# Performance work log

Hardware: AMD Instinct MI355X
Metric: run time of the kernel (lower is better)

The kernel has to match this reference:

```python
import math
import jax, jax.numpy as jnp
import numpy as np

# ---- module hyperparameters (from init_kwargs) ----
N_DELTA, N_THETA, N_GAMMA = 32, 64, 256
N_TOTAL = N_DELTA + N_THETA + N_GAMMA  # 352
N_DIMS = 1024
BATCH = 4096
N_STEPS = 32
DT = 0.01
COUPLING = 2.0
PAC = 0.3
EPS = 1e-6
TWO_PI = 2.0 * math.pi


def setup_inputs() -> dict:
    key = jax.random.key(0)
    k0, k1, k2 = jax.random.split(key, 3)
    x = jax.random.normal(k0, (BATCH, N_DIMS), dtype=jnp.float32)
    # xavier_uniform with gain=0.5 for Linear(n_dims, n_total, bias=False)
    bound = 0.5 * math.sqrt(6.0 / (N_DIMS + N_TOTAL))
    W_phase = jax.random.uniform(k1, (N_TOTAL, N_DIMS), jnp.float32, -bound, bound)
    W_amp = jax.random.uniform(k2, (N_TOTAL, N_DIMS), jnp.float32, -bound, bound)
    # natural angular frequencies per band: delta ~2Hz, theta ~6Hz, gamma ~40Hz
    omega = jnp.concatenate([
        jnp.full((N_DELTA,), TWO_PI * 2.0, jnp.float32),
        jnp.full((N_THETA,), TWO_PI * 6.0, jnp.float32),
        jnp.full((N_GAMMA,), TWO_PI * 40.0, jnp.float32),
    ])
    # block-diagonal intra-band Kuramoto coupling, K_ij = coupling_strength / n_band
    Kn = np.zeros((N_TOTAL, N_TOTAL), dtype=np.float32)
    o = 0
    for nb in (N_DELTA, N_THETA, N_GAMMA):
        Kn[o:o + nb, o:o + nb] = COUPLING / nb
        o += nb
    K = jnp.asarray(Kn)
    return {"x": x, "W_phase": W_phase, "W_amp": W_amp, "omega": omega, "K": K}


def reference(x, W_phase, W_amp, omega, K):
    # learned projections -> initial phase in [0, 2pi), amplitude clamped >= eps
    phase0 = (x @ W_phase.T) % TWO_PI                      # (B, n_total)
    amp0 = jnp.maximum(jnp.abs(x @ W_amp.T), EPS)          # (B, n_total)

    def step(carry, _):
        phase, amp = carry
        s, c = jnp.sin(phase), jnp.cos(phase)
        # sum_j K_ij sin(phi_j - phi_i) = cos(phi_i)*(K@sin)_i - sin(phi_i)*(K@cos)_i
        coup = c * (s @ K.T) - s * (c @ K.T)
        phase_n = (phase + DT * (omega + coup)) % TWO_PI
        d = phase_n[:, :N_DELTA]
        t = phase_n[:, N_DELTA:N_DELTA + N_THETA]
        mean_d = jnp.arctan2(jnp.sin(d).mean(-1), jnp.cos(d).mean(-1))  # (B,)
        mean_t = jnp.arctan2(jnp.sin(t).mean(-1), jnp.cos(t).mean(-1))  # (B,)
        B = phase.shape[0]
        mod = jnp.concatenate([
            jnp.zeros((B, N_DELTA), phase.dtype),
            jnp.broadcast_to((PAC * jnp.cos(mean_d))[:, None], (B, N_THETA)),
            jnp.broadcast_to((PAC * jnp.cos(mean_t))[:, None], (B, N_GAMMA)),
        ], axis=-1)
        amp_n = jnp.maximum(amp * (1.0 + DT * mod), EPS)
        return (phase_n, amp_n), None

    (final_phase, final_amp), _ = jax.lax.scan(step, (phase0, amp0), None, length=N_STEPS)
    return final_amp
```

## Files before the change

kernel.cpp:

```cpp
#include <hip/hip_runtime.h>

typedef float  f32x4 __attribute__((ext_vector_type(4)));
typedef short  s16x8 __attribute__((ext_vector_type(8)));
typedef _Float16 h2 __attribute__((ext_vector_type(2)));
typedef unsigned short u16;
typedef u16 u16x4 __attribute__((ext_vector_type(4)));

#define N_DIMS 1024
#define N_OSC  352
#define BATCH  4096
#define EPSV   1e-6f
#define INV2PI 0.15915494309189535f

__device__ __forceinline__ u16 f2bf(float f){
  unsigned u = __builtin_bit_cast(unsigned, f);
  u += 0x7FFFu + ((u >> 16) & 1u);
  return (u16)(u >> 16);
}

#define NX4 1048576
#define NW4 90112

__global__ __launch_bounds__(256) void convert_k(const f32x4* __restrict__ x,
    const f32x4* __restrict__ wp, const f32x4* __restrict__ wa,
    u16x4* __restrict__ xb, u16x4* __restrict__ wb){
  int i = blockIdx.x * 256 + threadIdx.x;
  f32x4 v; u16x4* dst;
  if (i < NX4) { v = x[i]; dst = xb + i; }
  else {
    int j = i - NX4;
    v = (j < NW4) ? wp[j] : wa[j - NW4];
    dst = wb + j;
  }
  u16x4 r;
  r[0]=f2bf(v[0]); r[1]=f2bf(v[1]); r[2]=f2bf(v[2]); r[3]=f2bf(v[3]);
  *dst = r;
}

__device__ __forceinline__ void gload16(const u16* g, u16* l){
  __builtin_amdgcn_global_load_lds(
      (const __attribute__((address_space(1))) unsigned int*)(g),
      (__attribute__((address_space(3))) unsigned int*)(l), 16, 0, 0);
}

__global__ __launch_bounds__(256) void gemm_k(const u16* __restrict__ xb,
    const u16* __restrict__ wb, float* __restrict__ phase0, float* __restrict__ amp0){
  __shared__ u16 lds[2][8192];
  const int tid = threadIdx.x;
  const int l   = tid & 63;
  const int w   = tid >> 6;
  const int m0  = blockIdx.y * 64;
  const int n0  = blockIdx.x * 64;

  const int srow = w*16 + (l >> 3);
  const int scol = (((l & 7) ^ (l >> 3)) * 8);
  const u16* ga = xb + (size_t)(m0 + srow) * N_DIMS + scol;
  const u16* gb = wb + (size_t)(n0 + srow) * N_DIMS + scol;

  #define STAGE(b, kt) { \
    const u16* gA = ga + (kt)*64; \
    const u16* gB = gb + (kt)*64; \
    gload16(gA,            &lds[b][w*1024]); \
    gload16(gA + 8*N_DIMS, &lds[b][w*1024 + 512]); \
    gload16(gB,            &lds[b][4096 + w*1024]); \
    gload16(gB + 8*N_DIMS, &lds[b][4096 + w*1024 + 512]); }

  const int rl = l & 15;
  const int q0 = l >> 4;
  const int sx = l & 7;
  const int wr = w >> 1, wc = w & 1;

  f32x4 acc[2][2] = {};
  STAGE(0, 0)
  __syncthreads();

  for (int kt = 0; kt < 16; kt++){
    const int cb = kt & 1;
    if (kt < 15) STAGE(cb^1, kt+1)
    s16x8 a[2][2], b[2][2];
    #pragma unroll
    for (int mi = 0; mi < 2; mi++)
    #pragma unroll
    for (int ks = 0; ks < 2; ks++){
      int off = (wr*32 + mi*16 + rl)*64 + (((ks*4 + q0) ^ sx) * 8);
      a[mi][ks] = *(const s16x8*)&lds[cb][off];
    }
    #pragma unroll
    for (int nj = 0; nj < 2; nj++)
    #pragma unroll
    for (int ks = 0; ks < 2; ks++){
      int off = 4096 + (wc*32 + nj*16 + rl)*64 + (((ks*4 + q0) ^ sx) * 8);
      b[nj][ks] = *(const s16x8*)&lds[cb][off];
    }
    #pragma unroll
    for (int ks = 0; ks < 2; ks++)
    #pragma unroll
    for (int mi = 0; mi < 2; mi++)
    #pragma unroll
    for (int nj = 0; nj < 2; nj++)
      acc[mi][nj] = __builtin_amdgcn_mfma_f32_16x16x32_bf16(a[mi][ks], b[nj][ks], acc[mi][nj], 0,0,0);
    __syncthreads();
  }
  #undef STAGE

  #pragma unroll
  for (int mi = 0; mi < 2; mi++)
  #pragma unroll
  for (int nj = 0; nj < 2; nj++){
    const int n = n0 + wc*32 + nj*16 + rl;
    #pragma unroll
    for (int r = 0; r < 4; r++){
      const int m = m0 + wr*32 + mi*16 + q0*4 + r;
      float v = acc[mi][nj][r];
      if (n < N_OSC) { float t = v * INV2PI; phase0[(size_t)m*N_OSC + n] = t - floorf(t); }
      else           { amp0[(size_t)m*N_OSC + (n - N_OSC)] = fmaxf(fabsf(v), EPSV); }
    }
  }
}

__device__ __forceinline__ int ibc(h2 v){ return __builtin_bit_cast(int, v); }
__device__ __forceinline__ h2  hbc(int v){ return __builtin_bit_cast(h2, v); }

__device__ __forceinline__ h2 rowsum16(h2 x){
  int v = ibc(x);
  v = ibc(hbc(v) + hbc(__builtin_amdgcn_mov_dpp(v, 0x121, 0xF, 0xF, true)));
  v = ibc(hbc(v) + hbc(__builtin_amdgcn_mov_dpp(v, 0x122, 0xF, 0xF, true)));
  v = ibc(hbc(v) + hbc(__builtin_amdgcn_mov_dpp(v, 0x124, 0xF, 0xF, true)));
  v = ibc(hbc(v) + hbc(__builtin_amdgcn_mov_dpp(v, 0x128, 0xF, 0xF, true)));
  return hbc(v);
}

__device__ __forceinline__ void updp(h2& s, h2& c, h2 cA, h2 sA, h2 GS, h2 GC){
  h2 e  = c*GS - s*GC;
  h2 s1 = s*cA + c*sA;
  h2 c1 = c*cA - s*sA;
  s = s1 + c1*e;
  c = c1 - s1*e;
}

__device__ __forceinline__ h2 splat2(_Float16 v){ h2 r; r[0]=v; r[1]=v; return r; }

__global__ __launch_bounds__(256) void iter_k(const float* __restrict__ phase0,
                                              float* __restrict__ amp){
  const int tid = threadIdx.x;
  const int l   = tid & 63;
  const int g   = l & 15;
  const int row = blockIdx.x*16 + (tid>>6)*4 + (l>>4);
  const size_t rb = (size_t)row * N_OSC;

  const h2 cAd = splat2((_Float16)0.99211470f), sAd = splat2((_Float16)0.12533323f);
  const h2 cAt = splat2((_Float16)0.92977649f), sAt = splat2((_Float16)0.36812455f);
  const h2 cAg = splat2((_Float16)-0.80901699f), sAg = splat2((_Float16)0.58778525f);
  const h2 kd = splat2((_Float16)6.25e-4f);
  const h2 kt = splat2((_Float16)3.125e-4f);
  const h2 kg = splat2((_Float16)7.8125e-5f);

  h2 sD, cD, sT[2], cT[2], sG[8], cG[8];
  {
    const float* pr = phase0 + rb;
    #define SCP(dstS, dstC, idx, p0, p1) { \
      float a0 = (p0), a1 = (p1); \
      dstS[idx][0] = (_Float16)__builtin_amdgcn_sinf(a0); \
      dstS[idx][1] = (_Float16)__builtin_amdgcn_sinf(a1); \
      dstC[idx][0] = (_Float16)__builtin_amdgcn_cosf(a0); \
      dstC[idx][1] = (_Float16)__builtin_amdgcn_cosf(a1); }
    {
      float2 d = *(const float2*)(pr + 2*g);
      sD[0] = (_Float16)__builtin_amdgcn_sinf(d.x);
      sD[1] = (_Float16)__builtin_amdgcn_sinf(d.y);
      cD[0] = (_Float16)__builtin_amdgcn_cosf(d.x);
      cD[1] = (_Float16)__builtin_amdgcn_cosf(d.y);
    }
    {
      float4 t = *(const float4*)(pr + 32 + 4*g);
      SCP(sT, cT, 0, t.x, t.y) SCP(sT, cT, 1, t.z, t.w)
    }
    #pragma unroll
    for (int i = 0; i < 4; i++){
      float4 v = *(const float4*)(pr + 96 + 16*g + 4*i);
      SCP(sG, cG, 2*i,   v.x, v.y) SCP(sG, cG, 2*i+1, v.z, v.w)
    }
    #undef SCP
  }

  h2 PD, PT, PG;
  #define REDUCE { \
    h2 pd; pd[0] = sD[0]+sD[1]; pd[1] = cD[0]+cD[1]; \
    h2 ts = sT[0]+sT[1], tc = cT[0]+cT[1]; \
    h2 pt; pt[0] = ts[0]+ts[1]; pt[1] = tc[0]+tc[1]; \
    h2 gs = ((sG[0]+sG[1])+(sG[2]+sG[3]))+((sG[4]+sG[5])+(sG[6]+sG[7])); \
    h2 gc = ((cG[0]+cG[1])+(cG[2]+cG[3]))+((cG[4]+cG[5])+(cG[6]+cG[7])); \
    h2 pg; pg[0] = gs[0]+gs[1]; pg[1] = gc[0]+gc[1]; \
    PD = rowsum16(pd); PT = rowsum16(pt); PG = rowsum16(pg); }

  REDUCE

  float Pth = 1.f, Pga = 1.f, mPth = 1.f, mPga = 1.f;
  for (int t = 0; t < 32; t++){
    h2 gd = PD * kd, gt = PT * kt, gg = PG * kg;
    h2 GSd = splat2(gd[0]), GCd = splat2(gd[1]);
    h2 GSt = splat2(gt[0]), GCt = splat2(gt[1]);
    h2 GSg = splat2(gg[0]), GCg = splat2(gg[1]);
    updp(sD, cD, cAd, sAd, GSd, GCd);
    updp(sT[0], cT[0], cAt, sAt, GSt, GCt);
    updp(sT[1], cT[1], cAt, sAt, GSt, GCt);
    #pragma unroll
    for (int i = 0; i < 8; i++) updp(sG[i], cG[i], cAg, sAg, GSg, GCg);
    REDUCE
    float Sd = (float)PD[0], Cd = (float)PD[1];
    float St = (float)PT[0], Ct = (float)PT[1];
    float ft = 1.f + 0.003f * Cd * __builtin_amdgcn_rsqf(Cd*Cd + Sd*Sd);
    float fg = 1.f + 0.003f * Ct * __builtin_amdgcn_rsqf(Ct*Ct + St*St);
    Pth *= ft; mPth = fminf(mPth, Pth);
    Pga *= fg; mPga = fminf(mPga, Pga);
  }
  #undef REDUCE

  const float cth = EPSV * Pth / mPth;
  const float cga = EPSV * Pga / mPga;
  {
    float4 a = *(const float4*)(amp + rb + 32 + 4*g);
    a.x = fmaxf(a.x*Pth, cth); a.y = fmaxf(a.y*Pth, cth);
    a.z = fmaxf(a.z*Pth, cth); a.w = fmaxf(a.w*Pth, cth);
    *(float4*)(amp + rb + 32 + 4*g) = a;
  }
  #pragma unroll
  for (int i = 0; i < 4; i++){
    float4 a = *(const float4*)(amp + rb + 96 + 16*g + 4*i);
    a.x = fmaxf(a.x*Pga, cga); a.y = fmaxf(a.y*Pga, cga);
    a.z = fmaxf(a.z*Pga, cga); a.w = fmaxf(a.w*Pga, cga);
    *(float4*)(amp + rb + 96 + 16*g + 4*i) = a;
  }
}

extern "C" void kernel_launch(void* const* d_in, const int* in_sizes, int n_in,
                              void* d_out, int out_size, void* d_ws, size_t ws_size,
                              hipStream_t stream){
  const float* x  = (const float*)d_in[0];
  const float* wp = (const float*)d_in[1];
  const float* wa = (const float*)d_in[2];
  float* out = (float*)d_out;
  char* ws = (char*)d_ws;
  u16* xb  = (u16*)(ws);
  u16* wb  = (u16*)(ws + 8388608);
  float* phase0 = (float*)(ws + 9830400);

  convert_k<<<4800, 256, 0, stream>>>((const f32x4*)x, (const f32x4*)wp, (const f32x4*)wa,
                                      (u16x4*)xb, (u16x4*)wb);
  gemm_k<<<dim3(11, 64), 256, 0, stream>>>(xb, wb, phase0, out);
  iter_k<<<256, 256, 0, stream>>>(phase0, out);
}
```

Baseline: 35.28 us.

## Widen GEMM N-tile to 128 and switch to 32x32x16 MFMA

The projection GEMM block tile grows from 64x64 to 64x128, and each wave now computes a 32x64 sub-tile using two 32x32x16 bf16 MFMAs instead of four 16x16x32 ones. The weight buffer is zero-padded to 768 rows so the wider tile divides evenly, and the epilogue skips tiles that fall entirely in padding. The aim is fewer LDS reads per FLOP, better A-tile reuse, and a smaller grid. The costs are more LDS per block, a slightly larger convert pass, and wasted MFMA work on the padded columns.

```diff
diff --git a/kernel.cpp b/kernel.cpp
--- a/kernel.cpp
+++ b/kernel.cpp
@@ -1,7 +1,8 @@
 #include <hip/hip_runtime.h>
 
-typedef float  f32x4 __attribute__((ext_vector_type(4)));
-typedef short  s16x8 __attribute__((ext_vector_type(8)));
+typedef float  f32x4  __attribute__((ext_vector_type(4)));
+typedef float  f32x16 __attribute__((ext_vector_type(16)));
+typedef short  s16x8  __attribute__((ext_vector_type(8)));
 typedef _Float16 h2 __attribute__((ext_vector_type(2)));
 typedef unsigned short u16;
 typedef u16 u16x4 __attribute__((ext_vector_type(4)));
@@ -29,8 +30,10 @@
   if (i < NX4) { v = x[i]; dst = xb + i; }
   else {
     int j = i - NX4;
-    v = (j < NW4) ? wp[j] : wa[j - NW4];
     dst = wb + j;
+    if (j < NW4)        v = wp[j];
+    else if (j < 2*NW4) v = wa[j - NW4];
+    else { u16x4 z = {0,0,0,0}; *dst = z; return; }
   }
   u16x4 r;
   r[0]=f2bf(v[0]); r[1]=f2bf(v[1]); r[2]=f2bf(v[2]); r[3]=f2bf(v[3]);
@@ -45,75 +48,72 @@
 
 __global__ __launch_bounds__(256) void gemm_k(const u16* __restrict__ xb,
     const u16* __restrict__ wb, float* __restrict__ phase0, float* __restrict__ amp0){
-  __shared__ u16 lds[2][8192];
+  __shared__ u16 lds[2][12288];
   const int tid = threadIdx.x;
   const int l   = tid & 63;
   const int w   = tid >> 6;
   const int m0  = blockIdx.y * 64;
-  const int n0  = blockIdx.x * 64;
-
-  const int srow = w*16 + (l >> 3);
-  const int scol = (((l & 7) ^ (l >> 3)) * 8);
-  const u16* ga = xb + (size_t)(m0 + srow) * N_DIMS + scol;
-  const u16* gb = wb + (size_t)(n0 + srow) * N_DIMS + scol;
+  const int n0  = blockIdx.x * 128;
+
+  const int sr8  = l >> 3;
+  const int scol = (((l & 7) ^ sr8) * 8);
+  const u16* ga = xb + (size_t)(m0 + w*16 + sr8) * N_DIMS + scol;
+  const u16* gb = wb + (size_t)(n0 + w*32 + sr8) * N_DIMS + scol;
 
   #define STAGE(b, kt) { \
     const u16* gA = ga + (kt)*64; \
     const u16* gB = gb + (kt)*64; \
-    gload16(gA,            &lds[b][w*1024]); \
-    gload16(gA + 8*N_DIMS, &lds[b][w*1024 + 512]); \
-    gload16(gB,            &lds[b][4096 + w*1024]); \
-    gload16(gB + 8*N_DIMS, &lds[b][4096 + w*1024 + 512]); }
-
-  const int rl = l & 15;
-  const int q0 = l >> 4;
-  const int sx = l & 7;
+    gload16(gA,             &lds[b][w*1024]); \
+    gload16(gA + 8*N_DIMS,  &lds[b][w*1024 + 512]); \
+    gload16(gB,             &lds[b][4096 + w*2048]); \
+    gload16(gB + 8*N_DIMS,  &lds[b][4096 + w*2048 + 512]); \
+    gload16(gB + 16*N_DIMS, &lds[b][4096 + w*2048 + 1024]); \
+    gload16(gB + 24*N_DIMS, &lds[b][4096 + w*2048 + 1536]); }
+
+  const int r31 = l & 31;
+  const int kh  = l >> 5;
   const int wr = w >> 1, wc = w & 1;
-
-  f32x4 acc[2][2] = {};
+  const int row_a = wr*32 + r31;
+  const int base_a = row_a*64;
+  const int sxa = row_a & 7;
+
+  f32x16 acc[2] = {};
   STAGE(0, 0)
   __syncthreads();
 
   for (int kt = 0; kt < 16; kt++){
     const int cb = kt & 1;
     if (kt < 15) STAGE(cb^1, kt+1)
-    s16x8 a[2][2], b[2][2];
-    #pragma unroll
-    for (int mi = 0; mi < 2; mi++)
-    #pragma unroll
-    for (int ks = 0; ks < 2; ks++){
-      int off = (wr*32 + mi*16 + rl)*64 + (((ks*4 + q0) ^ sx) * 8);
-      a[mi][ks] = *(const s16x8*)&lds[cb][off];
-    }
-    #pragma unroll
-    for (int nj = 0; nj < 2; nj++)
-    #pragma unroll
-    for (int ks = 0; ks < 2; ks++){
-      int off = 4096 + (wc*32 + nj*16 + rl)*64 + (((ks*4 + q0) ^ sx) * 8);
-      b[nj][ks] = *(const s16x8*)&lds[cb][off];
-    }
-    #pragma unroll
-    for (int ks = 0; ks < 2; ks++)
-    #pragma unroll
-    for (int mi = 0; mi < 2; mi++)
-    #pragma unroll
-    for (int nj = 0; nj < 2; nj++)
-      acc[mi][nj] = __builtin_amdgcn_mfma_f32_16x16x32_bf16(a[mi][ks], b[nj][ks], acc[mi][nj], 0,0,0);
+    #pragma unroll
+    for (int ks = 0; ks < 4; ks++){
+      const int s = ks*2 + kh;
+      s16x8 a = *(const s16x8*)&lds[cb][base_a + ((s ^ sxa) * 8)];
+      #pragma unroll
+      for (int nf = 0; nf < 2; nf++){
+        const int row_b = wc*64 + nf*32 + r31;
+        s16x8 b = *(const s16x8*)&lds[cb][4096 + row_b*64 + ((s ^ (row_b & 7)) * 8)];
+        acc[nf] = __builtin_amdgcn_mfma_f32_32x32x16_bf16(a, b, acc[nf], 0,0,0);
+      }
+    }
     __syncthreads();
   }
   #undef STAGE
 
   #pragma unroll
-  for (int mi = 0; mi < 2; mi++)
-  #pragma unroll
-  for (int nj = 0; nj < 2; nj++){
-    const int n = n0 + wc*32 + nj*16 + rl;
-    #pragma unroll
-    for (int r = 0; r < 4; r++){
-      const int m = m0 + wr*32 + mi*16 + q0*4 + r;
-      float v = acc[mi][nj][r];
-      if (n < N_OSC) { float t = v * INV2PI; phase0[(size_t)m*N_OSC + n] = t - floorf(t); }
-      else           { amp0[(size_t)m*N_OSC + (n - N_OSC)] = fmaxf(fabsf(v), EPSV); }
+  for (int nf = 0; nf < 2; nf++){
+    const int nb = n0 + wc*64 + nf*32;
+    if (nb >= 2*N_OSC) continue;
+    const bool isph = nb < N_OSC;
+    float* __restrict__ op = isph ? phase0 : amp0;
+    const int n = (isph ? nb : nb - N_OSC) + r31;
+    #pragma unroll
+    for (int r = 0; r < 16; r++){
+      const int m = m0 + wr*32 + (r&3) + 8*(r>>2) + 4*kh;
+      float v = acc[nf][r];
+      float res;
+      if (isph) { float t = v * INV2PI; res = t - floorf(t); }
+      else      { res = fmaxf(fabsf(v), EPSV); }
+      op[(size_t)m * N_OSC + n] = res;
     }
   }
 }
@@ -243,10 +243,10 @@
   char* ws = (char*)d_ws;
   u16* xb  = (u16*)(ws);
   u16* wb  = (u16*)(ws + 8388608);
-  float* phase0 = (float*)(ws + 9830400);
-
-  convert_k<<<4800, 256, 0, stream>>>((const f32x4*)x, (const f32x4*)wp, (const f32x4*)wa,
+  float* phase0 = (float*)(ws + 9961472);
+
+  convert_k<<<4864, 256, 0, stream>>>((const f32x4*)x, (const f32x4*)wp, (const f32x4*)wa,
                                       (u16x4*)xb, (u16x4*)wb);
-  gemm_k<<<dim3(11, 64), 256, 0, stream>>>(xb, wb, phase0, out);
+  gemm_k<<<dim3(6, 64), 256, 0, stream>>>(xb, wb, phase0, out);
   iter_k<<<256, 256, 0, stream>>>(phase0, out);
 }
```

New measurement: 35.41 us. Within noise of the previous version (+0.4%).

## Fuse fp32-to-bf16 conversion into GEMM loads with register-staged prefetch

Applied to the files above, without the earlier changes.

Removes the separate conversion kernel. The GEMM now loads fp32 x and weights directly into registers, converts them to bf16 with packed cvt instructions, and writes them to swizzled LDS. Register prefetch runs two k-tiles ahead, so the global loads overlap the MFMA work. The grid is also flattened to 704 blocks with a remapped block order for L2 locality. This saves a kernel launch and the bf16 round trip through global memory, but each GEMM block now reads twice the bytes (fp32) and carries more register pressure.

```diff
diff --git a/kernel.cpp b/kernel.cpp
--- a/kernel.cpp
+++ b/kernel.cpp
@@ -4,7 +4,6 @@
 typedef short  s16x8 __attribute__((ext_vector_type(8)));
 typedef _Float16 h2 __attribute__((ext_vector_type(2)));
 typedef unsigned short u16;
-typedef u16 u16x4 __attribute__((ext_vector_type(4)));
 
 #define N_DIMS 1024
 #define N_OSC  352
@@ -12,85 +11,81 @@
 #define EPSV   1e-6f
 #define INV2PI 0.15915494309189535f
 
-__device__ __forceinline__ u16 f2bf(float f){
-  unsigned u = __builtin_bit_cast(unsigned, f);
-  u += 0x7FFFu + ((u >> 16) & 1u);
-  return (u16)(u >> 16);
-}
-
-#define NX4 1048576
-#define NW4 90112
-
-__global__ __launch_bounds__(256) void convert_k(const f32x4* __restrict__ x,
-    const f32x4* __restrict__ wp, const f32x4* __restrict__ wa,
-    u16x4* __restrict__ xb, u16x4* __restrict__ wb){
-  int i = blockIdx.x * 256 + threadIdx.x;
-  f32x4 v; u16x4* dst;
-  if (i < NX4) { v = x[i]; dst = xb + i; }
-  else {
-    int j = i - NX4;
-    v = (j < NW4) ? wp[j] : wa[j - NW4];
-    dst = wb + j;
-  }
-  u16x4 r;
-  r[0]=f2bf(v[0]); r[1]=f2bf(v[1]); r[2]=f2bf(v[2]); r[3]=f2bf(v[3]);
-  *dst = r;
-}
-
-__device__ __forceinline__ void gload16(const u16* g, u16* l){
-  __builtin_amdgcn_global_load_lds(
-      (const __attribute__((address_space(1))) unsigned int*)(g),
-      (__attribute__((address_space(3))) unsigned int*)(l), 16, 0, 0);
-}
-
-__global__ __launch_bounds__(256) void gemm_k(const u16* __restrict__ xb,
-    const u16* __restrict__ wb, float* __restrict__ phase0, float* __restrict__ amp0){
+__device__ __forceinline__ void cvt_wr(const f32x4* rx, u16* b0, u16* b1){
+  unsigned v0,v1,v2,v3,v4,v5,v6,v7;
+  asm("v_cvt_pk_bf16_f32 %0, %1, %2" : "=v"(v0) : "v"(rx[0][0]), "v"(rx[0][1]));
+  asm("v_cvt_pk_bf16_f32 %0, %1, %2" : "=v"(v1) : "v"(rx[0][2]), "v"(rx[0][3]));
+  asm("v_cvt_pk_bf16_f32 %0, %1, %2" : "=v"(v2) : "v"(rx[1][0]), "v"(rx[1][1]));
+  asm("v_cvt_pk_bf16_f32 %0, %1, %2" : "=v"(v3) : "v"(rx[1][2]), "v"(rx[1][3]));
+  asm("v_cvt_pk_bf16_f32 %0, %1, %2" : "=v"(v4) : "v"(rx[2][0]), "v"(rx[2][1]));
+  asm("v_cvt_pk_bf16_f32 %0, %1, %2" : "=v"(v5) : "v"(rx[2][2]), "v"(rx[2][3]));
+  asm("v_cvt_pk_bf16_f32 %0, %1, %2" : "=v"(v6) : "v"(rx[3][0]), "v"(rx[3][1]));
+  asm("v_cvt_pk_bf16_f32 %0, %1, %2" : "=v"(v7) : "v"(rx[3][2]), "v"(rx[3][3]));
+  uint4 a; a.x=v0; a.y=v1; a.z=v2; a.w=v3;
+  uint4 b; b.x=v4; b.y=v5; b.z=v6; b.w=v7;
+  *(uint4*)b0 = a;
+  *(uint4*)b1 = b;
+}
+
+__global__ __launch_bounds__(256) void gemm_k(const float* __restrict__ xf,
+    const float* __restrict__ wpf, const float* __restrict__ waf,
+    float* __restrict__ phase0, float* __restrict__ amp0){
   __shared__ u16 lds[2][8192];
   const int tid = threadIdx.x;
   const int l   = tid & 63;
   const int w   = tid >> 6;
-  const int m0  = blockIdx.y * 64;
-  const int n0  = blockIdx.x * 64;
-
-  const int srow = w*16 + (l >> 3);
-  const int scol = (((l & 7) ^ (l >> 3)) * 8);
-  const u16* ga = xb + (size_t)(m0 + srow) * N_DIMS + scol;
-  const u16* gb = wb + (size_t)(n0 + srow) * N_DIMS + scol;
-
-  #define STAGE(b, kt) { \
-    const u16* gA = ga + (kt)*64; \
-    const u16* gB = gb + (kt)*64; \
-    gload16(gA,            &lds[b][w*1024]); \
-    gload16(gA + 8*N_DIMS, &lds[b][w*1024 + 512]); \
-    gload16(gB,            &lds[b][4096 + w*1024]); \
-    gload16(gB + 8*N_DIMS, &lds[b][4096 + w*1024 + 512]); }
+
+  const int bid = blockIdx.x;
+  const int s   = (bid & 7) * 88 + (bid >> 3);
+  const int m0  = (s / 11) * 64;
+  const int n0  = (s % 11) * 64;
+
+  const int r  = tid >> 2;
+  const int cq = tid & 3;
+  const float* ga = xf + (size_t)(m0 + r) * N_DIMS + cq * 16;
+  const int brow  = n0 + r;
+  const float* gb = ((brow < N_OSC) ? wpf + (size_t)brow * N_DIMS
+                                    : waf + (size_t)(brow - N_OSC) * N_DIMS) + cq * 16;
+  const int wa0 = r*64 + (((2*cq)   ^ (r&7)) * 8);
+  const int wa1 = r*64 + (((2*cq+1) ^ (r&7)) * 8);
+
+  f32x4 ra[4], rb[4];
+  #define LD(kt) { \
+    const float* pa = ga + (kt)*64; const float* pb = gb + (kt)*64; \
+    ra[0]=*(const f32x4*)(pa);    ra[1]=*(const f32x4*)(pa+4); \
+    ra[2]=*(const f32x4*)(pa+8);  ra[3]=*(const f32x4*)(pa+12); \
+    rb[0]=*(const f32x4*)(pb);    rb[1]=*(const f32x4*)(pb+4); \
+    rb[2]=*(const f32x4*)(pb+8);  rb[3]=*(const f32x4*)(pb+12); }
+  #define WR(b) { \
+    cvt_wr(ra, &lds[b][wa0],        &lds[b][wa1]); \
+    cvt_wr(rb, &lds[b][4096 + wa0], &lds[b][4096 + wa1]); }
 
   const int rl = l & 15;
   const int q0 = l >> 4;
-  const int sx = l & 7;
   const int wr = w >> 1, wc = w & 1;
 
   f32x4 acc[2][2] = {};
-  STAGE(0, 0)
+  LD(0)
+  WR(0)
+  LD(1)
   __syncthreads();
 
   for (int kt = 0; kt < 16; kt++){
     const int cb = kt & 1;
-    if (kt < 15) STAGE(cb^1, kt+1)
     s16x8 a[2][2], b[2][2];
     #pragma unroll
     for (int mi = 0; mi < 2; mi++)
     #pragma unroll
     for (int ks = 0; ks < 2; ks++){
-      int off = (wr*32 + mi*16 + rl)*64 + (((ks*4 + q0) ^ sx) * 8);
-      a[mi][ks] = *(const s16x8*)&lds[cb][off];
+      const int row = wr*32 + mi*16 + rl;
+      a[mi][ks] = *(const s16x8*)&lds[cb][row*64 + (((ks*4 + q0) ^ (row&7)) * 8)];
     }
     #pragma unroll
     for (int nj = 0; nj < 2; nj++)
     #pragma unroll
     for (int ks = 0; ks < 2; ks++){
-      int off = 4096 + (wc*32 + nj*16 + rl)*64 + (((ks*4 + q0) ^ sx) * 8);
-      b[nj][ks] = *(const s16x8*)&lds[cb][off];
+      const int row = wc*32 + nj*16 + rl;
+      b[nj][ks] = *(const s16x8*)&lds[cb][4096 + row*64 + (((ks*4 + q0) ^ (row&7)) * 8)];
     }
     #pragma unroll
     for (int ks = 0; ks < 2; ks++)
@@ -99,9 +94,14 @@
     #pragma unroll
     for (int nj = 0; nj < 2; nj++)
       acc[mi][nj] = __builtin_amdgcn_mfma_f32_16x16x32_bf16(a[mi][ks], b[nj][ks], acc[mi][nj], 0,0,0);
+    if (kt < 15){
+      WR(cb^1)
+      if (kt < 14) LD(kt+2)
+    }
     __syncthreads();
   }
-  #undef STAGE
+  #undef LD
+  #undef WR
 
   #pragma unroll
   for (int mi = 0; mi < 2; mi++)
@@ -109,9 +109,9 @@
   for (int nj = 0; nj < 2; nj++){
     const int n = n0 + wc*32 + nj*16 + rl;
     #pragma unroll
-    for (int r = 0; r < 4; r++){
-      const int m = m0 + wr*32 + mi*16 + q0*4 + r;
-      float v = acc[mi][nj][r];
+    for (int rg = 0; rg < 4; rg++){
+      const int m = m0 + wr*32 + mi*16 + q0*4 + rg;
+      float v = acc[mi][nj][rg];
       if (n < N_OSC) { float t = v * INV2PI; phase0[(size_t)m*N_OSC + n] = t - floorf(t); }
       else           { amp0[(size_t)m*N_OSC + (n - N_OSC)] = fmaxf(fabsf(v), EPSV); }
     }
@@ -240,13 +240,8 @@
   const float* wp = (const float*)d_in[1];
   const float* wa = (const float*)d_in[2];
   float* out = (float*)d_out;
-  char* ws = (char*)d_ws;
-  u16* xb  = (u16*)(ws);
-  u16* wb  = (u16*)(ws + 8388608);
-  float* phase0 = (float*)(ws + 9830400);
-
-  convert_k<<<4800, 256, 0, stream>>>((const f32x4*)x, (const f32x4*)wp, (const f32x4*)wa,
-                                      (u16x4*)xb, (u16x4*)wb);
-  gemm_k<<<dim3(11, 64), 256, 0, stream>>>(xb, wb, phase0, out);
+  float* phase0 = (float*)d_ws;
+
+  gemm_k<<<704, 256, 0, stream>>>(x, wp, wa, phase0, out);
   iter_k<<<256, 256, 0, stream>>>(phase0, out);
 }
```

New measurement: 39.92 us. 13.1% more time.
